# Kernel tuning notes

Measured on AMD Instinct MI355X. Metric: run time of the kernel, lower is better.

## Reference

```python
import jax, jax.numpy as jnp
import numpy as np

EMBED_DIM = 2048
NUM_HEADS = 32
NUM_SEQS = 8
SEQ_LEN = 1024
TOTAL_TOKENS = NUM_SEQS * SEQ_LEN


def setup_inputs() -> dict:
    key = jax.random.key(0)
    ks = jax.random.split(key, 9)
    E = EMBED_DIM
    std = 0.02
    return {
        "hidden_states": jax.random.normal(ks[0], (TOTAL_TOKENS, E), dtype=jnp.float32),
        "Wq": jax.random.normal(ks[1], (E, E), dtype=jnp.float32) * std,
        "bq": jax.random.normal(ks[2], (E,), dtype=jnp.float32) * std,
        "Wk": jax.random.normal(ks[3], (E, E), dtype=jnp.float32) * std,
        "bk": jax.random.normal(ks[4], (E,), dtype=jnp.float32) * std,
        "Wv": jax.random.normal(ks[5], (E, E), dtype=jnp.float32) * std,
        "bv": jax.random.normal(ks[6], (E,), dtype=jnp.float32) * std,
        "Wo": jax.random.normal(ks[7], (E, E), dtype=jnp.float32) * std,
        "bo": jax.random.normal(ks[8], (E,), dtype=jnp.float32) * std,
        "seq_len": SEQ_LEN,
    }


def reference(hidden_states, Wq, bq, Wk, bk, Wv, bv, Wo, bo, seq_len):
    # OPTAttention (has_cache=False): block-diagonal causal attention over
    # packed ragged sequences; here all NUM_SEQS sequences have length seq_len,
    # so the block-diagonal mask is exactly per-sequence causal attention.
    T, E = hidden_states.shape
    H = NUM_HEADS
    D = E // H
    B = T // seq_len
    scaling = D ** -0.5

    # torch nn.Linear: y = x @ W.T + b
    q = hidden_states @ Wq.T + bq
    k = hidden_states @ Wk.T + bk
    v = hidden_states @ Wv.T + bv

    q = q.reshape(B, seq_len, H, D)
    k = k.reshape(B, seq_len, H, D)
    v = v.reshape(B, seq_len, H, D)

    # [B, H, S, S] attention scores (xformers applies scale to q@k.T)
    scores = jnp.einsum("bqhd,bkhd->bhqk", q, k) * scaling
    causal = jnp.tril(jnp.ones((seq_len, seq_len), dtype=bool))
    scores = jnp.where(causal[None, None, :, :], scores, jnp.finfo(scores.dtype).min)
    probs = jax.nn.softmax(scores, axis=-1)

    attn = jnp.einsum("bhqk,bkhd->bqhd", probs, v)  # [B, S, H, D]
    attn = attn.reshape(T, E)
    return attn @ Wo.T + bo
```

## Files before the change

kernel.cpp:

```cpp
#include <hip/hip_runtime.h>
#include <hip/hip_bf16.h>

typedef __bf16 bf16_t;
typedef __bf16 bf16x8 __attribute__((ext_vector_type(8)));
typedef __bf16 bf16x4 __attribute__((ext_vector_type(4)));
typedef float f32x4 __attribute__((ext_vector_type(4)));
typedef float f32x16 __attribute__((ext_vector_type(16)));
typedef unsigned short u16x8 __attribute__((ext_vector_type(8)));
typedef unsigned int u32x4 __attribute__((ext_vector_type(4)));

#define T_TOK 8192
#define E_DIM 2048
#define NHEAD 32
#define SEQLEN 1024
#define NSEQ 8
#define LDQ 6144

#if __has_builtin(__builtin_amdgcn_exp2f)
#define EXP2F(x) __builtin_amdgcn_exp2f(x)
#else
#define EXP2F(x) exp2f(x)
#endif

static __device__ inline unsigned cvtpk_bf16(float lo, float hi) {
    unsigned r;
    asm("v_cvt_pk_bf16_f32 %0, %1, %2" : "=v"(r) : "v"(lo), "v"(hi));
    return r;
}

static __device__ inline void plswap(unsigned &x, unsigned &y, bool lo_half) {
#if __has_builtin(__builtin_amdgcn_permlane32_swap)
    auto r = __builtin_amdgcn_permlane32_swap(x, y, false, false);
    x = r[0]; y = r[1];
#else
    unsigned xs = __shfl_xor(x, 32), ys = __shfl_xor(y, 32);
    unsigned nx = lo_half ? x : ys;
    unsigned ny = lo_half ? xs : y;
    x = nx; y = ny;
#endif
}

__global__ void cvt_f32_bf16(const float* __restrict__ in, bf16_t* __restrict__ out, int n4) {
    int idx = blockIdx.x * blockDim.x + threadIdx.x;
    int stride = gridDim.x * blockDim.x;
    for (int i = idx; i < n4; i += stride) {
        const float4 v = reinterpret_cast<const float4*>(in)[i];
        bf16x4 o;
        o[0] = (bf16_t)v.x; o[1] = (bf16_t)v.y; o[2] = (bf16_t)v.z; o[3] = (bf16_t)v.w;
        reinterpret_cast<bf16x4*>(out)[i] = o;
    }
}

template<bool OUT_BF16>
__global__ __launch_bounds__(512, 2)
void gemm256p(const bf16_t* __restrict__ A, const bf16_t* __restrict__ B,
              const float* __restrict__ b0, const float* __restrict__ b1,
              const float* __restrict__ b2, void* __restrict__ Cout,
              int M, int N, float qs, int qlim) {
    constexpr int K = 2048;
    constexpr int NK = K / 32;
    __shared__ alignas(16) unsigned char lds[131072];
    const int tid = threadIdx.x;
    const int wid = tid >> 6, l = tid & 63;
    const int cpx = gridDim.x >> 3;
    const int wg = (blockIdx.x & 7) * cpx + (blockIdx.x >> 3);
    const int nbm = M >> 8;
    const int bm = wg % nbm, bn = wg / nbm;
    const int wrow = (wid >> 2) * 128, wcol = (wid & 3) * 64;
    const int lr = l & 15, lg = l >> 4;

    f32x4 acc[8][4] = {};

    const bf16_t* aBase = A + (size_t)(bm * 256) * K;
    const bf16_t* bBase = B + (size_t)(bn * 256) * K;
    const int sr = l >> 2;
    const int sc = (l & 3) * 16;

    auto stageA = [&](int t) {
        unsigned char* base = lds + (t & 3) * 32768;
#pragma unroll
        for (int c = 0; c < 2; ++c) {
            const int chunk = wid * 2 + c;
            const int r = chunk * 16 + sr;
            const int cb = sc ^ (((r >> 1) & 3) << 4);
            __builtin_amdgcn_global_load_lds(
                (const __attribute__((address_space(1))) void*)(aBase + (size_t)r * K + t * 32 + (cb >> 1)),
                (__attribute__((address_space(3))) void*)(base + chunk * 1024), 16, 0, 0);
        }
    };
    auto stageB = [&](int t) {
        unsigned char* base = lds + (t & 3) * 32768 + 16384;
#pragma unroll
        for (int c = 0; c < 2; ++c) {
            const int chunk = wid * 2 + c;
            const int r = chunk * 16 + sr;
            const int cb = sc ^ (((r >> 1) & 3) << 4);
            __builtin_amdgcn_global_load_lds(
                (const __attribute__((address_space(1))) void*)(bBase + (size_t)r * K + t * 32 + (cb >> 1)),
                (__attribute__((address_space(3))) void*)(base + chunk * 1024), 16, 0, 0);
        }
    };

    stageA(0); stageB(0); stageA(1); stageB(1); stageA(2); stageB(2);
    asm volatile("s_waitcnt vmcnt(8)" ::: "memory");
    __builtin_amdgcn_s_barrier();

    for (int t = 0; t < NK; ++t) {
        const unsigned char* Ab = lds + (t & 3) * 32768;
        const unsigned char* Bb = Ab + 16384;
        bf16x8 af[8], bfv[4];
#pragma unroll
        for (int m = 0; m < 4; ++m) {
            const int r = wrow + m * 16 + lr;
            af[m] = *reinterpret_cast<const bf16x8*>(Ab + r * 64 + ((lg * 16) ^ (((r >> 1) & 3) << 4)));
        }
#pragma unroll
        for (int n = 0; n < 4; ++n) {
            const int r = wcol + n * 16 + lr;
            bfv[n] = *reinterpret_cast<const bf16x8*>(Bb + r * 64 + ((lg * 16) ^ (((r >> 1) & 3) << 4)));
        }
        if (t + 3 < NK) stageA(t + 3);
        __builtin_amdgcn_s_barrier();
        asm volatile("s_waitcnt lgkmcnt(0)" ::: "memory");
        __builtin_amdgcn_sched_barrier(0);
        __builtin_amdgcn_s_setprio(1);
#pragma unroll
        for (int m = 0; m < 4; ++m)
#pragma unroll
            for (int n = 0; n < 4; ++n)
                acc[m][n] = __builtin_amdgcn_mfma_f32_16x16x32_bf16(af[m], bfv[n], acc[m][n], 0, 0, 0);
        __builtin_amdgcn_s_setprio(0);
        __builtin_amdgcn_s_barrier();
#pragma unroll
        for (int m = 4; m < 8; ++m) {
            const int r = wrow + m * 16 + lr;
            af[m] = *reinterpret_cast<const bf16x8*>(Ab + r * 64 + ((lg * 16) ^ (((r >> 1) & 3) << 4)));
        }
        if (t + 3 < NK) stageB(t + 3);
        __builtin_amdgcn_s_barrier();
        asm volatile("s_waitcnt lgkmcnt(0)" ::: "memory");
        __builtin_amdgcn_sched_barrier(0);
        __builtin_amdgcn_s_setprio(1);
#pragma unroll
        for (int m = 4; m < 8; ++m)
#pragma unroll
            for (int n = 0; n < 4; ++n)
                acc[m][n] = __builtin_amdgcn_mfma_f32_16x16x32_bf16(af[m], bfv[n], acc[m][n], 0, 0, 0);
        __builtin_amdgcn_s_setprio(0);
        if (t == NK - 1) break;
        if (t <= NK - 4)      asm volatile("s_waitcnt vmcnt(8)" ::: "memory");
        else if (t == NK - 3) asm volatile("s_waitcnt vmcnt(4)" ::: "memory");
        else                  asm volatile("s_waitcnt vmcnt(0)" ::: "memory");
        __builtin_amdgcn_s_barrier();
    }

    const int r0 = bm * 256 + wrow + lg * 4;
    const int c0 = bn * 256 + wcol + lr;
#pragma unroll
    for (int n = 0; n < 4; ++n) {
        const int cc = c0 + n * 16;
        const float bias = (cc < 2048) ? b0[cc] : (cc < 4096 ? b1[cc - 2048] : b2[cc - 4096]);
        const float sc2 = (cc < qlim) ? qs : 1.0f;
#pragma unroll
        for (int m = 0; m < 8; ++m)
#pragma unroll
            for (int j = 0; j < 4; ++j) {
                const int rr = r0 + m * 16 + j;
                const float v = (acc[m][n][j] + bias) * sc2;
                if (OUT_BF16) ((bf16_t*)Cout)[(size_t)rr * N + cc] = (bf16_t)v;
                else          ((float*)Cout)[(size_t)rr * N + cc] = v;
            }
    }
}

__global__ __launch_bounds__(512, 2)
void attn_fwd3(const bf16_t* __restrict__ QKV, bf16_t* __restrict__ Og) {
    const int orig = blockIdx.x;
    const int id = (orig & 7) * 64 + (orig >> 3);
    const int grp = id >> 1;
    const int pairIdx = id & 1;
    const int h = grp & 31;
    const int sq = grp >> 5;

    const int tid = threadIdx.x;
    const int w = tid >> 6;
    const int l = tid & 63;
    const int ll = l & 31;
    const int hi = l >> 5;
    const bool lo_half = (hi == 0);

    __shared__ alignas(16) unsigned char lds[65536];

    const bf16_t* Qg = QKV;
    const bf16_t* Kg = QKV + 2048;
    const bf16_t* Vg = QKV + 4096;
    const size_t kvbase = (size_t)(sq * SEQLEN) * LDQ + h * 64;

    bf16x8 vr0, vr1;
    const int vk0 = l * 2;
    const int vd0 = w * 8;

    auto stageK = [&](int kt, int buf) {
#pragma unroll
        for (int c = 0; c < 2; ++c) {
            const int o = (w * 2 + c) * 1024 + l * 16;
            const int r = o >> 7;
            const int swb = (o & 127) ^ ((r & 7) << 4);
            const bf16_t* src = Kg + kvbase + (size_t)(kt * 128 + r) * LDQ + (swb >> 1);
            __builtin_amdgcn_global_load_lds(
                (const __attribute__((address_space(1))) void*)src,
                (__attribute__((address_space(3))) void*)(lds + buf * 16384 + (w * 2 + c) * 1024),
                16, 0, 0);
        }
    };
    auto loadV = [&](int kt) {
        const bf16_t* vp = Vg + kvbase + (size_t)(kt * 128 + vk0) * LDQ + vd0;
        vr0 = *reinterpret_cast<const bf16x8*>(vp);
        vr1 = *reinterpret_cast<const bf16x8*>(vp + LDQ);
    };
    auto writeV = [&](int buf) {
        u16x8 s0 = __builtin_bit_cast(u16x8, vr0);
        u16x8 s1 = __builtin_bit_cast(u16x8, vr1);
        unsigned char* vb = lds + 32768 + buf * 16384;
#pragma unroll
        for (int e = 0; e < 8; ++e) {
            const int d = vd0 + e;
            unsigned off = (unsigned)(d * 256 + vk0 * 2);
            off ^= ((unsigned)((d ^ (d >> 4)) & 15)) << 4;
            *reinterpret_cast<unsigned*>(vb + off) = (unsigned)s0[e] | ((unsigned)s1[e] << 16);
        }
    };

    const unsigned ksw = (unsigned)((l & 7) << 4);
    const unsigned kbase = (unsigned)(ll * 128 + hi * 16);

#pragma unroll 1
    for (int seg = 0; seg < 2; ++seg) {
        const int qt = pairIdx ? (seg ? 2 : 1) : (seg ? 3 : 0);

        const int q_glob = qt * 256 + w * 32 + ll;
        const bf16_t* qp = Qg + (size_t)(sq * SEQLEN + q_glob) * LDQ + h * 64 + hi * 8;
        bf16x8 qf[4];
#pragma unroll
        for (int dc = 0; dc < 4; ++dc)
            qf[dc] = *reinterpret_cast<const bf16x8*>(qp + dc * 16);

        const int nkt = 2 * qt + 2;
        const int q_wave_max = qt * 256 + w * 32 + 31;

        f32x16 oac[2] = {};
        float mrun = -3.0e38f, lsum = 0.f;

        stageK(0, 0);
        loadV(0);
        writeV(0);
        __syncthreads();

        int cur = 0;
        for (int kt = 0; kt < nkt; ++kt) {
            const bool notlast = (kt + 1 < nkt);
            if (notlast) { stageK(kt + 1, cur ^ 1); loadV(kt + 1); }

            if (kt * 128 <= q_wave_max) {
                const unsigned char* Kcur = lds + cur * 16384;
                const unsigned char* Vcur = lds + 32768 + cur * 16384;

                f32x16 st[4];
#pragma unroll
                for (int kh = 0; kh < 4; ++kh) {
                    f32x16 acc = {};
#pragma unroll
                    for (int dc = 0; dc < 4; ++dc) {
                        const unsigned off = (kbase + (unsigned)(kh * 4096 + dc * 32)) ^ ksw;
                        const bf16x8 ka = *reinterpret_cast<const bf16x8*>(Kcur + off);
                        acc = __builtin_amdgcn_mfma_f32_32x32x16_bf16(ka, qf[dc], acc, 0, 0, 0);
                    }
                    st[kh] = acc;
                }

                if (kt >= 2 * qt) {
#pragma unroll
                    for (int kh = 0; kh < 4; ++kh)
#pragma unroll
                        for (int r = 0; r < 16; ++r) {
                            const int kg = kt * 128 + kh * 32 + (r & 3) + 8 * (r >> 2) + 4 * hi;
                            if (kg > q_glob) st[kh][r] = -3.0e38f;
                        }
                }

                float tm = -3.0e38f;
#pragma unroll
                for (int kh = 0; kh < 4; ++kh)
#pragma unroll
                    for (int r = 0; r < 16; ++r) tm = fmaxf(tm, st[kh][r]);
                tm = fmaxf(tm, __shfl_xor(tm, 32));

                if (!__all(tm <= mrun + 8.0f)) {
                    const float mnew = fmaxf(mrun, tm);
                    const float rsc = EXP2F(mrun - mnew);
                    mrun = mnew;
                    lsum *= rsc;
#pragma unroll
                    for (int dh = 0; dh < 2; ++dh)
#pragma unroll
                        for (int r = 0; r < 16; ++r) oac[dh][r] *= rsc;
                }

                float ps = 0.f;
#pragma unroll
                for (int kh = 0; kh < 4; ++kh)
#pragma unroll
                    for (int r = 0; r < 16; ++r) {
                        const float p = EXP2F(st[kh][r] - mrun);
                        st[kh][r] = p;
                        ps += p;
                    }
                ps += __shfl_xor(ps, 32);
                lsum += ps;

                bf16x8 pf[8];
#pragma unroll
                for (int kh = 0; kh < 4; ++kh)
#pragma unroll
                    for (int hc = 0; hc < 2; ++hc) {
                        const int b0i = hc * 8;
                        unsigned a  = cvtpk_bf16(st[kh][b0i + 0], st[kh][b0i + 1]);
                        unsigned b  = cvtpk_bf16(st[kh][b0i + 4], st[kh][b0i + 5]);
                        unsigned a2 = cvtpk_bf16(st[kh][b0i + 2], st[kh][b0i + 3]);
                        unsigned b2 = cvtpk_bf16(st[kh][b0i + 6], st[kh][b0i + 7]);
                        plswap(a, b, lo_half);
                        plswap(a2, b2, lo_half);
                        u32x4 words = { a, a2, b, b2 };
                        pf[kh * 2 + hc] = __builtin_bit_cast(bf16x8, words);
                    }

#pragma unroll
                for (int dh = 0; dh < 2; ++dh) {
                    const int d = dh * 32 + ll;
                    const unsigned vsw = ((unsigned)((d ^ (d >> 4)) & 15)) << 4;
                    const unsigned vbb = (unsigned)(d * 256 + hi * 16);
#pragma unroll
                    for (int kc = 0; kc < 8; ++kc) {
                        const unsigned off = (vbb + (unsigned)(kc * 32)) ^ vsw;
                        const bf16x8 vfr = *reinterpret_cast<const bf16x8*>(Vcur + off);
                        oac[dh] = __builtin_amdgcn_mfma_f32_32x32x16_bf16(vfr, pf[kc], oac[dh], 0, 0, 0);
                    }
                }
            }

            if (notlast) writeV(cur ^ 1);
            __syncthreads();
            cur ^= 1;
        }

        const float inv = 1.0f / lsum;
        bf16_t* op = Og + (size_t)(sq * SEQLEN + q_glob) * E_DIM + h * 64;
#pragma unroll
        for (int dh = 0; dh < 2; ++dh)
#pragma unroll
            for (int rq = 0; rq < 4; ++rq) {
                const int d0 = dh * 32 + 8 * rq + 4 * hi;
                bf16x4 ov;
#pragma unroll
                for (int j = 0; j < 4; ++j)
                    ov[j] = (bf16_t)(oac[dh][rq * 4 + j] * inv);
                *reinterpret_cast<bf16x4*>(op + d0) = ov;
            }
    }
}

extern "C" void kernel_launch(void* const* d_in, const int* in_sizes, int n_in,
                              void* d_out, int out_size, void* d_ws, size_t ws_size,
                              hipStream_t stream) {
    const float* hid = (const float*)d_in[0];
    const float* Wq  = (const float*)d_in[1];
    const float* bq  = (const float*)d_in[2];
    const float* Wk  = (const float*)d_in[3];
    const float* bk  = (const float*)d_in[4];
    const float* Wv  = (const float*)d_in[5];
    const float* bv  = (const float*)d_in[6];
    const float* Wo  = (const float*)d_in[7];
    const float* bo  = (const float*)d_in[8];
    float* out = (float*)d_out;

    const size_t TE = (size_t)T_TOK * E_DIM;
    const size_t EE = (size_t)E_DIM * E_DIM;

    bf16_t* ws   = (bf16_t*)d_ws;
    bf16_t* hidB = ws;
    bf16_t* qkvB = ws + TE;
    bf16_t* Wcat = qkvB + 3 * TE;
    bf16_t* WoB  = Wcat + 3 * EE;

    cvt_f32_bf16<<<2048, 256, 0, stream>>>(hid, hidB, (int)(TE / 4));
    cvt_f32_bf16<<<1024, 256, 0, stream>>>(Wq, Wcat, (int)(EE / 4));
    cvt_f32_bf16<<<1024, 256, 0, stream>>>(Wk, Wcat + EE, (int)(EE / 4));
    cvt_f32_bf16<<<1024, 256, 0, stream>>>(Wv, Wcat + 2 * EE, (int)(EE / 4));
    cvt_f32_bf16<<<1024, 256, 0, stream>>>(Wo, WoB, (int)(EE / 4));

    const float QSCALE = 0.125f * 1.4426950408889634f;

    gemm256p<true><<<dim3((T_TOK / 256) * (LDQ / 256)), 512, 0, stream>>>(
        hidB, Wcat, bq, bk, bv, qkvB, T_TOK, LDQ, QSCALE, 2048);

    attn_fwd3<<<dim3(512), 512, 0, stream>>>(qkvB, hidB);

    gemm256p<false><<<dim3((T_TOK / 256) * (E_DIM / 256)), 512, 0, stream>>>(
        hidB, WoB, bo, bo, bo, out, T_TOK, E_DIM, 1.0f, 0);
}
```

Before: 412.5 us.

## Simplify GEMM main loop to a single barrier per K-step with merged staging

```diff
diff --git a/kernel.cpp b/kernel.cpp
--- a/kernel.cpp
+++ b/kernel.cpp
@@ -53,7 +53,7 @@
 
 template<bool OUT_BF16>
 __global__ __launch_bounds__(512, 2)
-void gemm256p(const bf16_t* __restrict__ A, const bf16_t* __restrict__ B,
+void gemm256r(const bf16_t* __restrict__ A, const bf16_t* __restrict__ B,
               const float* __restrict__ b0, const float* __restrict__ b1,
               const float* __restrict__ b2, void* __restrict__ Cout,
               int M, int N, float qs, int qlim) {
@@ -76,7 +76,7 @@
     const int sr = l >> 2;
     const int sc = (l & 3) * 16;
 
-    auto stageA = [&](int t) {
+    auto stage = [&](int t) {
         unsigned char* base = lds + (t & 3) * 32768;
 #pragma unroll
         for (int c = 0; c < 2; ++c) {
@@ -86,71 +86,42 @@
             __builtin_amdgcn_global_load_lds(
                 (const __attribute__((address_space(1))) void*)(aBase + (size_t)r * K + t * 32 + (cb >> 1)),
                 (__attribute__((address_space(3))) void*)(base + chunk * 1024), 16, 0, 0);
-        }
-    };
-    auto stageB = [&](int t) {
-        unsigned char* base = lds + (t & 3) * 32768 + 16384;
-#pragma unroll
-        for (int c = 0; c < 2; ++c) {
-            const int chunk = wid * 2 + c;
-            const int r = chunk * 16 + sr;
-            const int cb = sc ^ (((r >> 1) & 3) << 4);
             __builtin_amdgcn_global_load_lds(
                 (const __attribute__((address_space(1))) void*)(bBase + (size_t)r * K + t * 32 + (cb >> 1)),
-                (__attribute__((address_space(3))) void*)(base + chunk * 1024), 16, 0, 0);
+                (__attribute__((address_space(3))) void*)(base + 16384 + chunk * 1024), 16, 0, 0);
         }
     };
 
-    stageA(0); stageB(0); stageA(1); stageB(1); stageA(2); stageB(2);
+    stage(0); stage(1); stage(2);
     asm volatile("s_waitcnt vmcnt(8)" ::: "memory");
     __builtin_amdgcn_s_barrier();
 
     for (int t = 0; t < NK; ++t) {
+        if (t + 3 < NK) stage(t + 3);
         const unsigned char* Ab = lds + (t & 3) * 32768;
         const unsigned char* Bb = Ab + 16384;
-        bf16x8 af[8], bfv[4];
-#pragma unroll
-        for (int m = 0; m < 4; ++m) {
-            const int r = wrow + m * 16 + lr;
-            af[m] = *reinterpret_cast<const bf16x8*>(Ab + r * 64 + ((lg * 16) ^ (((r >> 1) & 3) << 4)));
-        }
+        bf16x8 bfv[4], af[8];
 #pragma unroll
         for (int n = 0; n < 4; ++n) {
             const int r = wcol + n * 16 + lr;
             bfv[n] = *reinterpret_cast<const bf16x8*>(Bb + r * 64 + ((lg * 16) ^ (((r >> 1) & 3) << 4)));
         }
-        if (t + 3 < NK) stageA(t + 3);
-        __builtin_amdgcn_s_barrier();
-        asm volatile("s_waitcnt lgkmcnt(0)" ::: "memory");
-        __builtin_amdgcn_sched_barrier(0);
-        __builtin_amdgcn_s_setprio(1);
-#pragma unroll
-        for (int m = 0; m < 4; ++m)
-#pragma unroll
-            for (int n = 0; n < 4; ++n)
-                acc[m][n] = __builtin_amdgcn_mfma_f32_16x16x32_bf16(af[m], bfv[n], acc[m][n], 0, 0, 0);
-        __builtin_amdgcn_s_setprio(0);
-        __builtin_amdgcn_s_barrier();
-#pragma unroll
-        for (int m = 4; m < 8; ++m) {
+#pragma unroll
+        for (int m = 0; m < 8; ++m) {
             const int r = wrow + m * 16 + lr;
             af[m] = *reinterpret_cast<const bf16x8*>(Ab + r * 64 + ((lg * 16) ^ (((r >> 1) & 3) << 4)));
         }
-        if (t + 3 < NK) stageB(t + 3);
-        __builtin_amdgcn_s_barrier();
-        asm volatile("s_waitcnt lgkmcnt(0)" ::: "memory");
-        __builtin_amdgcn_sched_barrier(0);
         __builtin_amdgcn_s_setprio(1);
 #pragma unroll
-        for (int m = 4; m < 8; ++m)
+        for (int m = 0; m < 8; ++m)
 #pragma unroll
             for (int n = 0; n < 4; ++n)
                 acc[m][n] = __builtin_amdgcn_mfma_f32_16x16x32_bf16(af[m], bfv[n], acc[m][n], 0, 0, 0);
         __builtin_amdgcn_s_setprio(0);
         if (t == NK - 1) break;
-        if (t <= NK - 4)      asm volatile("s_waitcnt vmcnt(8)" ::: "memory");
-        else if (t == NK - 3) asm volatile("s_waitcnt vmcnt(4)" ::: "memory");
-        else                  asm volatile("s_waitcnt vmcnt(0)" ::: "memory");
+        if (t + 3 < NK)      asm volatile("s_waitcnt vmcnt(8)" ::: "memory");
+        else if (t + 2 < NK) asm volatile("s_waitcnt vmcnt(4)" ::: "memory");
+        else                 asm volatile("s_waitcnt vmcnt(0)" ::: "memory");
         __builtin_amdgcn_s_barrier();
     }
 
@@ -400,11 +371,11 @@
 
     const float QSCALE = 0.125f * 1.4426950408889634f;
 
-    gemm256p<true><<<dim3((T_TOK / 256) * (LDQ / 256)), 512, 0, stream>>>(
+    gemm256r<true><<<dim3((T_TOK / 256) * (LDQ / 256)), 512, 0, stream>>>(
         hidB, Wcat, bq, bk, bv, qkvB, T_TOK, LDQ, QSCALE, 2048);
 
     attn_fwd3<<<dim3(512), 512, 0, stream>>>(qkvB, hidB);
 
-    gemm256p<false><<<dim3((T_TOK / 256) * (E_DIM / 256)), 512, 0, stream>>>(
+    gemm256r<false><<<dim3((T_TOK / 256) * (E_DIM / 256)), 512, 0, stream>>>(
         hidB, WoB, bo, bo, bo, out, T_TOK, E_DIM, 1.0f, 0);
 }
```

Result: no change. 410.4 us (-0.5%).
